# Kernel tuning notes

Measured on AMD Instinct MI355X. Metric: run time of the kernel, lower is better.

## Reference

```python
import jax, jax.numpy as jnp
import numpy as np

EPS = 1e-8
N_GENRES = 10


def gelu(x):
    return jax.nn.gelu(x, approximate=False)  # torch nn.GELU default = exact erf


def setup_inputs() -> dict:
    B, IN_DIM, DIM = 4096, 512, 1024
    key = jax.random.key(0)
    ks = jax.random.split(key, 14)
    inp = {
        "noise": jax.random.normal(ks[0], (B, IN_DIM), dtype=jnp.float32),  # unused (dead arg in original)
        "genre_batch": jax.random.randint(ks[1], (B,), 0, N_GENRES),
        "z": jax.random.normal(ks[2], (B, IN_DIM), dtype=jnp.float32),  # reparam noise for torch.normal
        # per-genre distribution params
        "mu_table": jax.random.normal(ks[3], (N_GENRES, IN_DIM), dtype=jnp.float32),
        "sigma_table": jax.random.normal(ks[4], (N_GENRES, IN_DIM), dtype=jnp.float32),
        # shared MLP: in_dim -> dim -> dim
        "Ws1": jax.random.normal(ks[5], (IN_DIM, DIM), dtype=jnp.float32) * (1.0 / np.sqrt(IN_DIM)),
        "bs1": jnp.zeros((DIM,), dtype=jnp.float32),
        "Ws2": jax.random.normal(ks[6], (DIM, DIM), dtype=jnp.float32) * (1.0 / np.sqrt(DIM)),
        "bs2": jnp.zeros((DIM,), dtype=jnp.float32),
        # 10 unshared expert MLPs: dim -> dim -> dim
        "We1": jax.random.normal(ks[7], (N_GENRES, DIM, DIM), dtype=jnp.float32) * (1.0 / np.sqrt(DIM)),
        "be1": jnp.zeros((N_GENRES, DIM), dtype=jnp.float32),
        "We2": jax.random.normal(ks[8], (N_GENRES, DIM, DIM), dtype=jnp.float32) * (1.0 / np.sqrt(DIM)),
        "be2": jnp.zeros((N_GENRES, DIM), dtype=jnp.float32),
    }
    return inp


def reference(noise, genre_batch, z, mu_table, sigma_table,
              Ws1, bs1, Ws2, bs2, We1, be1, We2, be2):
    # per-sample gather of genre mu/sigma, then reparameterized normal sample
    mu = mu_table[genre_batch]                              # [B, in_dim]
    std = jnp.abs(sigma_table[genre_batch]) + EPS           # [B, in_dim]
    noise_genre = mu + std * z                              # ~ Normal(mu, std)

    # shared MLP
    s = gelu(noise_genre @ Ws1 + bs1)                       # [B, dim]
    s = gelu(s @ Ws2 + bs2)                                 # [B, dim]

    # per-sample expert dispatch: compute all 10 experts densely, select by genre
    h = gelu(jnp.einsum('bd,edh->ebh', s, We1) + be1[:, None, :])   # [E, B, dim]
    o = jnp.einsum('ebh,eho->ebo', h, We2) + be2[:, None, :]        # [E, B, dim]
    out = o[genre_batch, jnp.arange(s.shape[0])]            # [B, dim]
    return out
```

## Files before the change

kernel.cpp:

```cpp
#include <hip/hip_runtime.h>
#include <hip/hip_bf16.h>

typedef __bf16 bf16;
typedef __bf16 bf16x8 __attribute__((ext_vector_type(8)));
typedef float floatx4 __attribute__((ext_vector_type(4)));

#define B_ROWS 4096
#define IN_DIM 512
#define DIM 1024
#define NG 10

__device__ __forceinline__ float geluf(float x) {
    return 0.5f * x * (1.0f + erff(x * 0.70710678118654752f));
}

__device__ __forceinline__ void async16(void* lds, const void* g) {
    __builtin_amdgcn_global_load_lds(
        (const __attribute__((address_space(1))) unsigned int*)g,
        (__attribute__((address_space(3))) unsigned int*)lds, 16, 0, 0);
}

__global__ void prep_kernel(const int* __restrict__ genre,
                            const float* __restrict__ z,
                            const float* __restrict__ mu_t,
                            const float* __restrict__ sg_t,
                            bf16* __restrict__ ng) {
    const int t = blockIdx.x * 256 + threadIdx.x;
    const int row = t >> 6;
    const int c0 = (t & 63) * 8;
    const int g = genre[row];
    const float* zp = z + (size_t)row * IN_DIM + c0;
    const float* mp = mu_t + (size_t)g * IN_DIM + c0;
    const float* sp = sg_t + (size_t)g * IN_DIM + c0;
    floatx4 z0 = *(const floatx4*)zp, z1 = *(const floatx4*)(zp + 4);
    floatx4 m0 = *(const floatx4*)mp, m1 = *(const floatx4*)(mp + 4);
    floatx4 s0 = *(const floatx4*)sp, s1 = *(const floatx4*)(sp + 4);
    bf16x8 o;
#pragma unroll
    for (int i = 0; i < 4; i++) {
        o[i] = (bf16)(m0[i] + (fabsf(s0[i]) + 1e-8f) * z0[i]);
        o[i + 4] = (bf16)(m1[i] + (fabsf(s1[i]) + 1e-8f) * z1[i]);
    }
    *(bf16x8*)(ng + (size_t)row * IN_DIM + c0) = o;
}

__global__ void bucket_kernel(const int* __restrict__ genre,
                              int* __restrict__ counts,
                              int* __restrict__ offsets,
                              int* __restrict__ row_ids) {
    __shared__ int hist[NG];
    __shared__ int base[NG];
    const int tid = threadIdx.x;
    if (tid < NG) hist[tid] = 0;
    __syncthreads();
    int g[4];
#pragma unroll
    for (int i = 0; i < 4; i++) {
        g[i] = genre[tid + i * 1024];
        atomicAdd(&hist[g[i]], 1);
    }
    __syncthreads();
    if (tid == 0) {
        int acc = 0;
        for (int e = 0; e < NG; e++) {
            base[e] = acc;
            counts[e] = hist[e];
            offsets[e] = acc;
            acc += hist[e];
        }
        offsets[NG] = acc;
    }
    __syncthreads();
    if (tid < NG) hist[tid] = base[tid];
    __syncthreads();
#pragma unroll
    for (int i = 0; i < 4; i++) {
        int pos = atomicAdd(&hist[g[i]], 1);
        row_ids[pos] = tid + i * 1024;
    }
}

__global__ void transpose_all_kernel(const float* __restrict__ Ws1,
                                     const float* __restrict__ Ws2,
                                     const float* __restrict__ We1,
                                     const float* __restrict__ We2,
                                     bf16* __restrict__ WT1,
                                     bf16* __restrict__ WT2,
                                     bf16* __restrict__ WE1T,
                                     bf16* __restrict__ WE2T) {
    int b = blockIdx.x;
    const float* src;
    bf16* dst;
    int R, ty;
    if (b < 128) {
        src = Ws1; dst = WT1; R = 512; ty = b >> 4; b &= 15;
    } else if (b < 384) {
        b -= 128; src = Ws2; dst = WT2; R = 1024; ty = b >> 4; b &= 15;
    } else if (b < 2944) {
        b -= 384;
        int e = b >> 8; b &= 255;
        src = We1 + (size_t)e * DIM * DIM;
        dst = WE1T + (size_t)e * DIM * DIM;
        R = 1024; ty = b >> 4; b &= 15;
    } else {
        b -= 2944;
        int e = b >> 8; b &= 255;
        src = We2 + (size_t)e * DIM * DIM;
        dst = WE2T + (size_t)e * DIM * DIM;
        R = 1024; ty = b >> 4; b &= 15;
    }
    const int r0 = ty * 64, c0 = b * 64;
    __shared__ float T[64 * 64];
    const int tid = threadIdx.x;
#pragma unroll
    for (int i = 0; i < 4; i++) {
        const int s = i * 256 + tid;
        const int r = s >> 4;
        const int cv = s & 15;
        floatx4 v = *(const floatx4*)(src + (size_t)(r0 + r) * 1024 + c0 + cv * 4);
        *(floatx4*)(T + r * 64 + ((cv ^ (r >> 3)) * 4)) = v;
    }
    __syncthreads();
#pragma unroll
    for (int i = 0; i < 2; i++) {
        const int s = i * 256 + tid;
        const int oc = s >> 3;
        const int og = s & 7;
        const int cg = oc >> 2, o = oc & 3;
        bf16x8 v;
#pragma unroll
        for (int t = 0; t < 8; t++) {
            const int r = og * 8 + t;
            v[t] = (bf16)T[r * 64 + ((cg ^ (r >> 3)) * 4) + o];
        }
        *(bf16x8*)(dst + (size_t)(c0 + oc) * R + r0 + og * 8) = v;
    }
}

template <bool EXPERT, bool GATHER_A, bool SCATTER_C, bool GELU, typename CT>
__global__ __launch_bounds__(256, 4) void gemm_kernel(
    const bf16* __restrict__ A, const bf16* __restrict__ BT,
    const float* __restrict__ bias, CT* __restrict__ Cmat,
    int M, int N, int K,
    const int* __restrict__ row_ids, const int* __restrict__ offsets,
    const int* __restrict__ counts) {
    int off = 0, cnt = M;
    if (EXPERT) {
        const int g = blockIdx.z;
        cnt = counts[g];
        if ((int)blockIdx.y * 128 >= cnt) return;
        off = offsets[g];
        BT += (size_t)g * N * K;
        bias += (size_t)g * N;
    }
    const int m_start = blockIdx.y * 128;
    const int n0 = blockIdx.x * 64;

    constexpr int BK = 128;
    __shared__ bf16 As[128 * BK];
    __shared__ bf16 Bs[64 * BK];

    const int tid = threadIdx.x;
    const int lane = tid & 63;
    const int wave = tid >> 6;
    const int wrow = (wave >> 1) * 64;
    const int wcol = (wave & 1) * 32;
    const int quad = lane >> 4;
    const int l16 = lane & 15;

    const bf16* a_src[8];
    bf16* a_dst[8];
#pragma unroll
    for (int i = 0; i < 8; i++) {
        const int s = i * 256 + tid;
        const int row = s >> 4;
        const int col = ((s & 15) ^ (row & 15)) * 8;
        a_dst[i] = As + (i * 256 + wave * 64) * 8;
        int p = m_start + row;
        size_t arow;
        if (EXPERT) {
            int pp = off + min(p, cnt - 1);
            arow = GATHER_A ? (size_t)row_ids[pp] : (size_t)pp;
        } else {
            arow = (size_t)p;
        }
        a_src[i] = A + arow * (size_t)K + col;
    }
    const bf16* b_src[4];
    bf16* b_dst[4];
#pragma unroll
    for (int i = 0; i < 4; i++) {
        const int s = i * 256 + tid;
        const int row = s >> 4;
        const int col = ((s & 15) ^ (row & 15)) * 8;
        b_dst[i] = Bs + (i * 256 + wave * 64) * 8;
        b_src[i] = BT + (size_t)(n0 + row) * K + col;
    }

    floatx4 acc[4][2];
#pragma unroll
    for (int i = 0; i < 4; i++)
#pragma unroll
        for (int j = 0; j < 2; j++)
#pragma unroll
            for (int r = 0; r < 4; r++) acc[i][j][r] = 0.0f;

    const int nK = K / BK;
    for (int kt = 0; kt < nK; kt++) {
        const int kbase = kt * BK;
#pragma unroll
        for (int i = 0; i < 8; i++) async16(a_dst[i], a_src[i] + kbase);
#pragma unroll
        for (int i = 0; i < 4; i++) async16(b_dst[i], b_src[i] + kbase);
        __syncthreads();
#pragma unroll
        for (int ks = 0; ks < 4; ks++) {
            bf16x8 af[4], bfr[2];
            const int cb = ks * 4 + quad;
#pragma unroll
            for (int i = 0; i < 4; i++) {
                const int r = wrow + i * 16 + l16;
                af[i] = *(const bf16x8*)(As + (r * 16 + (cb ^ (r & 15))) * 8);
            }
#pragma unroll
            for (int j = 0; j < 2; j++) {
                const int n = wcol + j * 16 + l16;
                bfr[j] = *(const bf16x8*)(Bs + (n * 16 + (cb ^ (n & 15))) * 8);
            }
#pragma unroll
            for (int i = 0; i < 4; i++)
#pragma unroll
                for (int j = 0; j < 2; j++)
                    acc[i][j] = __builtin_amdgcn_mfma_f32_16x16x32_bf16(
                        af[i], bfr[j], acc[i][j], 0, 0, 0);
        }
        __syncthreads();
    }

#pragma unroll
    for (int j = 0; j < 2; j++) {
        const int n = n0 + wcol + j * 16 + l16;
        const float bv = bias[n];
#pragma unroll
        for (int i = 0; i < 4; i++) {
            const int rbase = wrow + i * 16 + quad * 4;
#pragma unroll
            for (int r = 0; r < 4; r++) {
                const int p = m_start + rbase + r;
                if (EXPERT && p >= cnt) continue;
                float v = acc[i][j][r] + bv;
                if (GELU) v = geluf(v);
                size_t drow;
                if (EXPERT) {
                    const int pp = off + p;
                    drow = SCATTER_C ? (size_t)row_ids[pp] : (size_t)pp;
                } else {
                    drow = (size_t)p;
                }
                Cmat[drow * (size_t)N + n] = (CT)v;
            }
        }
    }
}

extern "C" void kernel_launch(void* const* d_in, const int* in_sizes, int n_in,
                              void* d_out, int out_size, void* d_ws,
                              size_t ws_size, hipStream_t stream) {
    const int* genre = (const int*)d_in[1];
    const float* z = (const float*)d_in[2];
    const float* mu_t = (const float*)d_in[3];
    const float* sg_t = (const float*)d_in[4];
    const float* Ws1 = (const float*)d_in[5];
    const float* bs1 = (const float*)d_in[6];
    const float* Ws2 = (const float*)d_in[7];
    const float* bs2 = (const float*)d_in[8];
    const float* We1 = (const float*)d_in[9];
    const float* be1 = (const float*)d_in[10];
    const float* We2 = (const float*)d_in[11];
    const float* be2 = (const float*)d_in[12];
    float* out = (float*)d_out;

    char* w = (char*)d_ws;
    int* counts = (int*)w;
    int* offsets = (int*)(w + 256);
    int* row_ids = (int*)(w + 1024);
    char* wb = w + (64 << 10);
    bf16* ng = (bf16*)wb;
    bf16* hp = (bf16*)wb;
    bf16* s1 = (bf16*)(wb + ((size_t)4 << 20));
    bf16* s2 = (bf16*)(wb + ((size_t)12 << 20));
    bf16* WT1 = (bf16*)(wb + ((size_t)20 << 20));
    bf16* WT2 = WT1 + (size_t)IN_DIM * DIM;
    bf16* WE1T = WT2 + (size_t)DIM * DIM;
    bf16* WE2T = WE1T + (size_t)NG * DIM * DIM;

    bucket_kernel<<<1, 1024, 0, stream>>>(genre, counts, offsets, row_ids);
    prep_kernel<<<B_ROWS * IN_DIM / 8 / 256, 256, 0, stream>>>(genre, z, mu_t,
                                                               sg_t, ng);
    transpose_all_kernel<<<5504, 256, 0, stream>>>(Ws1, Ws2, We1, We2, WT1,
                                                   WT2, WE1T, WE2T);

    gemm_kernel<false, false, false, true, bf16>
        <<<dim3(DIM / 64, B_ROWS / 128), 256, 0, stream>>>(
            ng, WT1, bs1, s1, B_ROWS, DIM, IN_DIM, nullptr, nullptr, nullptr);
    gemm_kernel<false, false, false, true, bf16>
        <<<dim3(DIM / 64, B_ROWS / 128), 256, 0, stream>>>(
            s1, WT2, bs2, s2, B_ROWS, DIM, DIM, nullptr, nullptr, nullptr);
    gemm_kernel<true, true, false, true, bf16>
        <<<dim3(DIM / 64, B_ROWS / 128, NG), 256, 0, stream>>>(
            s2, WE1T, be1, hp, B_ROWS, DIM, DIM, row_ids, offsets, counts);
    gemm_kernel<true, false, true, false, float>
        <<<dim3(DIM / 64, B_ROWS / 128, NG), 256, 0, stream>>>(
            hp, WE2T, be2, out, B_ROWS, DIM, DIM, row_ids, offsets, counts);
}
```

Baseline: 254.1 us.

## Double-buffer GEMM LDS tiles with async prefetch and enlarge transpose tiles

The GEMM main loop now uses two LDS buffers with BK=64, prefetching the next K tile through global_load_lds while the current one is consumed. It replaces the full __syncthreads with a vmcnt wait plus a raw barrier, so global-load latency can overlap MFMA work. The transpose kernel now handles two 64x64 tiles per block and launches half as many blocks. Launch bounds drop to 3 blocks per CU, and the partial vmcnt wait relies on load ordering that is easy to get wrong.

After: 250.0 us. No clear change (-1.6%).

```diff
diff --git a/kernel.cpp b/kernel.cpp
--- a/kernel.cpp
+++ b/kernel.cpp
@@ -19,6 +19,8 @@
         (const __attribute__((address_space(1))) unsigned int*)g,
         (__attribute__((address_space(3))) unsigned int*)lds, 16, 0, 0);
 }
+#define WAIT_VM(N) __builtin_amdgcn_s_waitcnt(0x0F70 | (N))
+#define BARRIER() __builtin_amdgcn_s_barrier()
 
 __global__ void prep_kernel(const int* __restrict__ genre,
                             const float* __restrict__ z,
@@ -91,54 +93,60 @@
     int b = blockIdx.x;
     const float* src;
     bf16* dst;
-    int R, ty;
-    if (b < 128) {
-        src = Ws1; dst = WT1; R = 512; ty = b >> 4; b &= 15;
-    } else if (b < 384) {
-        b -= 128; src = Ws2; dst = WT2; R = 1024; ty = b >> 4; b &= 15;
-    } else if (b < 2944) {
-        b -= 384;
-        int e = b >> 8; b &= 255;
+    int R;
+    if (b < 64) {
+        src = Ws1; dst = WT1; R = 512;
+    } else if (b < 192) {
+        b -= 64; src = Ws2; dst = WT2; R = 1024;
+    } else if (b < 1472) {
+        b -= 192;
+        int e = b >> 7; b &= 127;
         src = We1 + (size_t)e * DIM * DIM;
         dst = WE1T + (size_t)e * DIM * DIM;
-        R = 1024; ty = b >> 4; b &= 15;
+        R = 1024;
     } else {
-        b -= 2944;
-        int e = b >> 8; b &= 255;
+        b -= 1472;
+        int e = b >> 7; b &= 127;
         src = We2 + (size_t)e * DIM * DIM;
         dst = WE2T + (size_t)e * DIM * DIM;
-        R = 1024; ty = b >> 4; b &= 15;
-    }
-    const int r0 = ty * 64, c0 = b * 64;
-    __shared__ float T[64 * 64];
+        R = 1024;
+    }
+    const int r0 = (b >> 4) * 128;
+    const int c0 = (b & 15) * 64;
+    __shared__ float T[2][64 * 64];
     const int tid = threadIdx.x;
 #pragma unroll
-    for (int i = 0; i < 4; i++) {
-        const int s = i * 256 + tid;
-        const int r = s >> 4;
-        const int cv = s & 15;
-        floatx4 v = *(const floatx4*)(src + (size_t)(r0 + r) * 1024 + c0 + cv * 4);
-        *(floatx4*)(T + r * 64 + ((cv ^ (r >> 3)) * 4)) = v;
-    }
-    __syncthreads();
-#pragma unroll
-    for (int i = 0; i < 2; i++) {
-        const int s = i * 256 + tid;
-        const int oc = s >> 3;
-        const int og = s & 7;
-        const int cg = oc >> 2, o = oc & 3;
-        bf16x8 v;
-#pragma unroll
-        for (int t = 0; t < 8; t++) {
-            const int r = og * 8 + t;
-            v[t] = (bf16)T[r * 64 + ((cg ^ (r >> 3)) * 4) + o];
-        }
-        *(bf16x8*)(dst + (size_t)(c0 + oc) * R + r0 + og * 8) = v;
-    }
+    for (int t = 0; t < 2; t++)
+#pragma unroll
+        for (int i = 0; i < 4; i++) {
+            const int s = i * 256 + tid;
+            const int r = s >> 4;
+            const int cv = s & 15;
+            floatx4 v = *(const floatx4*)(src + (size_t)(r0 + t * 64 + r) * 1024 +
+                                          c0 + cv * 4);
+            *(floatx4*)(T[t] + r * 64 + ((cv ^ (r >> 3)) * 4)) = v;
+        }
+    __syncthreads();
+#pragma unroll
+    for (int t = 0; t < 2; t++)
+#pragma unroll
+        for (int i = 0; i < 2; i++) {
+            const int s = i * 256 + tid;
+            const int oc = s >> 3;
+            const int og = s & 7;
+            const int cg = oc >> 2, o = oc & 3;
+            bf16x8 v;
+#pragma unroll
+            for (int u = 0; u < 8; u++) {
+                const int r = og * 8 + u;
+                v[u] = (bf16)T[t][r * 64 + ((cg ^ (r >> 3)) * 4) + o];
+            }
+            *(bf16x8*)(dst + (size_t)(c0 + oc) * R + r0 + t * 64 + og * 8) = v;
+        }
 }
 
 template <bool EXPERT, bool GATHER_A, bool SCATTER_C, bool GELU, typename CT>
-__global__ __launch_bounds__(256, 4) void gemm_kernel(
+__global__ __launch_bounds__(256, 3) void gemm_kernel(
     const bf16* __restrict__ A, const bf16* __restrict__ BT,
     const float* __restrict__ bias, CT* __restrict__ Cmat,
     int M, int N, int K,
@@ -156,9 +164,9 @@
     const int m_start = blockIdx.y * 128;
     const int n0 = blockIdx.x * 64;
 
-    constexpr int BK = 128;
-    __shared__ bf16 As[128 * BK];
-    __shared__ bf16 Bs[64 * BK];
+    constexpr int BK = 64;
+    __shared__ bf16 As[2][128 * BK];
+    __shared__ bf16 Bs[2][64 * BK];
 
     const int tid = threadIdx.x;
     const int lane = tid & 63;
@@ -168,14 +176,12 @@
     const int quad = lane >> 4;
     const int l16 = lane & 15;
 
-    const bf16* a_src[8];
-    bf16* a_dst[8];
-#pragma unroll
-    for (int i = 0; i < 8; i++) {
+    const bf16* a_src[4];
+#pragma unroll
+    for (int i = 0; i < 4; i++) {
         const int s = i * 256 + tid;
-        const int row = s >> 4;
-        const int col = ((s & 15) ^ (row & 15)) * 8;
-        a_dst[i] = As + (i * 256 + wave * 64) * 8;
+        const int row = s >> 3;
+        const int col = ((s & 7) ^ (row & 7)) * 8;
         int p = m_start + row;
         size_t arow;
         if (EXPERT) {
@@ -186,16 +192,15 @@
         }
         a_src[i] = A + arow * (size_t)K + col;
     }
-    const bf16* b_src[4];
-    bf16* b_dst[4];
-#pragma unroll
-    for (int i = 0; i < 4; i++) {
+    const bf16* b_src[2];
+#pragma unroll
+    for (int i = 0; i < 2; i++) {
         const int s = i * 256 + tid;
-        const int row = s >> 4;
-        const int col = ((s & 15) ^ (row & 15)) * 8;
-        b_dst[i] = Bs + (i * 256 + wave * 64) * 8;
+        const int row = s >> 3;
+        const int col = ((s & 7) ^ (row & 7)) * 8;
         b_src[i] = BT + (size_t)(n0 + row) * K + col;
     }
+    const int ldsbase = wave * 64 * 8;
 
     floatx4 acc[4][2];
 #pragma unroll
@@ -206,26 +211,35 @@
             for (int r = 0; r < 4; r++) acc[i][j][r] = 0.0f;
 
     const int nK = K / BK;
+#pragma unroll
+    for (int i = 0; i < 4; i++) async16(&As[0][i * 2048 + ldsbase], a_src[i]);
+#pragma unroll
+    for (int i = 0; i < 2; i++) async16(&Bs[0][i * 2048 + ldsbase], b_src[i]);
+
     for (int kt = 0; kt < nK; kt++) {
-        const int kbase = kt * BK;
-#pragma unroll
-        for (int i = 0; i < 8; i++) async16(a_dst[i], a_src[i] + kbase);
-#pragma unroll
-        for (int i = 0; i < 4; i++) async16(b_dst[i], b_src[i] + kbase);
-        __syncthreads();
-#pragma unroll
-        for (int ks = 0; ks < 4; ks++) {
+        const int cur = kt & 1, nxt = cur ^ 1;
+        const int kn = (kt + 1 < nK) ? (kt + 1) * BK : 0;
+#pragma unroll
+        for (int i = 0; i < 4; i++)
+            async16(&As[nxt][i * 2048 + ldsbase], a_src[i] + kn);
+#pragma unroll
+        for (int i = 0; i < 2; i++)
+            async16(&Bs[nxt][i * 2048 + ldsbase], b_src[i] + kn);
+        WAIT_VM(6);
+        BARRIER();
+#pragma unroll
+        for (int ks = 0; ks < 2; ks++) {
             bf16x8 af[4], bfr[2];
             const int cb = ks * 4 + quad;
 #pragma unroll
             for (int i = 0; i < 4; i++) {
                 const int r = wrow + i * 16 + l16;
-                af[i] = *(const bf16x8*)(As + (r * 16 + (cb ^ (r & 15))) * 8);
+                af[i] = *(const bf16x8*)(&As[cur][(r * 8 + (cb ^ (r & 7))) * 8]);
             }
 #pragma unroll
             for (int j = 0; j < 2; j++) {
                 const int n = wcol + j * 16 + l16;
-                bfr[j] = *(const bf16x8*)(Bs + (n * 16 + (cb ^ (n & 15))) * 8);
+                bfr[j] = *(const bf16x8*)(&Bs[cur][(n * 8 + (cb ^ (n & 7))) * 8]);
             }
 #pragma unroll
             for (int i = 0; i < 4; i++)
@@ -234,7 +248,7 @@
                     acc[i][j] = __builtin_amdgcn_mfma_f32_16x16x32_bf16(
                         af[i], bfr[j], acc[i][j], 0, 0, 0);
         }
-        __syncthreads();
+        BARRIER();
     }
 
 #pragma unroll
@@ -295,9 +309,8 @@
     bf16* WE2T = WE1T + (size_t)NG * DIM * DIM;
 
     bucket_kernel<<<1, 1024, 0, stream>>>(genre, counts, offsets, row_ids);
-    prep_kernel<<<B_ROWS * IN_DIM / 8 / 256, 256, 0, stream>>>(genre, z, mu_t,
-                                                               sg_t, ng);
-    transpose_all_kernel<<<5504, 256, 0, stream>>>(Ws1, Ws2, We1, We2, WT1,
+    prep_kernel<<<1024, 256, 0, stream>>>(genre, z, mu_t, sg_t, ng);
+    transpose_all_kernel<<<2752, 256, 0, stream>>>(Ws1, Ws2, We1, We2, WT1,
                                                    WT2, WE1T, WE2T);
 
     gemm_kernel<false, false, false, true, bf16>
```
